# Performance work log

Measured on AMD Instinct MI355X. Metric: run time of the kernel, lower is better.

The kernel has to match this reference:

```python
import jax, jax.numpy as jnp
import numpy as np

def mexican_hat(z):
    z2 = z * z
    return (1.0 - z2) * jnp.exp(-0.5 * z2)

def setup_inputs() -> dict:
    key = jax.random.key(0)
    k1, k2 = jax.random.split(key)
    B, N, D = 8192, 512, 64
    x = jax.random.normal(k1, (B, D), dtype=jnp.float32)
    centers = jax.random.normal(k2, (N, D), dtype=jnp.float32)
    scales = jnp.ones((N, D), dtype=jnp.float32)
    return {"x": x, "centers": centers, "scales": scales}

def reference(x, centers, scales):
    # x: (B, D); centers/scales: (N, D)
    z = (x[:, None, :] - centers[None, :, :]) / scales[None, :, :]  # (B, N, D)
    psi = mexican_hat(z)
    h = jnp.prod(psi, axis=2)  # (B, N)
    return h
```

## Files before the change

kernel.cpp:

```cpp
#include <hip/hip_runtime.h>
#include <hip/hip_bf16.h>


#define DD 64
#define BSTRIP 8

typedef float v2f __attribute__((ext_vector_type(2)));

__global__ __launch_bounds__(256)
void prep(const float* __restrict__ c, const float* __restrict__ s,
          float4* __restrict__ pp, int N) {
    int i = blockIdx.x * 256 + threadIdx.x;
    if (i < (DD / 2) * N) {
        int dp = i / N, n = i - dp * N;
        float r0 = 1.0f / s[n * DD + 2 * dp];
        float r1 = 1.0f / s[n * DD + 2 * dp + 1];
        pp[i] = make_float4(c[n * DD + 2 * dp] * r0,
                            c[n * DD + 2 * dp + 1] * r1, r0, r1);
    }
}

__global__ __launch_bounds__(256, 4)
void wavelet_kernel(const float* __restrict__ x,
                    const float4* __restrict__ pp,
                    float* __restrict__ out, int B, int N) {
    int t = threadIdx.x;
    int lane = t & 63;
    int wv = __builtin_amdgcn_readfirstlane(t >> 6);
    int n = blockIdx.y * 64 + lane;
    int b0 = (blockIdx.x * 4 + wv) * BSTRIP;

    const float4* pcol = pp + n;

    float acc[BSTRIP];
#pragma unroll
    for (int bi = 0; bi < BSTRIP; ++bi) acc[bi] = 1.0f;

#pragma unroll
    for (int h = 0; h < 4; ++h) {
        v2f cp[8], rs[8];
#pragma unroll
        for (int i = 0; i < 8; ++i) {
            float4 q = pcol[(size_t)(h * 8 + i) * N];
            cp[i] = (v2f){q.x, q.y};
            rs[i] = (v2f){q.z, q.w};
        }

#pragma unroll
        for (int bi = 0; bi < BSTRIP; ++bi) {
            const float4* xq =
                (const float4*)(x + (size_t)(b0 + bi) * DD + h * 16);
            float4 X0 = xq[0];
            float4 X1 = xq[1];
            float4 X2 = xq[2];
            float4 X3 = xq[3];
            float xs[16] = {X0.x, X0.y, X0.z, X0.w,
                            X1.x, X1.y, X1.z, X1.w,
                            X2.x, X2.y, X2.z, X2.w,
                            X3.x, X3.y, X3.z, X3.w};
            v2f p  = {1.0f, 1.0f};
            v2f s2 = {0.0f, 0.0f};
#pragma unroll
            for (int k = 0; k < 8; ++k) {
                v2f xv = {xs[2 * k], xs[2 * k + 1]};
                v2f z = __builtin_elementwise_fma(xv, rs[k], -cp[k]);
                v2f w = z * z;
                p = __builtin_elementwise_fma(-w, p, p);
                s2 += w;
            }
            acc[bi] *= (p.x * p.y) *
                       __builtin_exp2f(-0.72134752f * (s2.x + s2.y));
        }
    }

#pragma unroll
    for (int bi = 0; bi < BSTRIP; ++bi)
        out[(size_t)(b0 + bi) * N + n] = acc[bi];
}

extern "C" void kernel_launch(void* const* d_in, const int* in_sizes, int n_in,
                              void* d_out, int out_size, void* d_ws, size_t ws_size,
                              hipStream_t stream) {
    const float* x = (const float*)d_in[0];
    const float* c = (const float*)d_in[1];
    const float* s = (const float*)d_in[2];
    float* out = (float*)d_out;

    int B = in_sizes[0] / DD;
    int N = in_sizes[1] / DD;

    float4* pp = (float4*)d_ws;

    int total = (DD / 2) * N;
    prep<<<(total + 255) / 256, 256, 0, stream>>>(c, s, pp, N);

    dim3 grid(B / (4 * BSTRIP), N / 64);
    wavelet_kernel<<<grid, 256, 0, stream>>>(x, pp, out, B, N);
}
```

Measured before the change: 85.11 us.

## Stage center/scale params through double-buffered LDS via global_load_lds

Each block now loads the precomputed center/scale pairs through a double-buffered shared-memory stage, filled with global_load_lds, and shares them across its four waves. Previously each wave loaded all 32 float4s per lane straight from global memory. The dimension loop is split into eight chunks of eight dims, each prefetching the next chunk. This removes duplicate global loads and register pressure but adds a __syncthreads per chunk and issues exp2 twice as often (once per 8 dims instead of 16).

Result: slower. 185.4 us (+117.9%).

```diff
diff --git a/kernel.cpp b/kernel.cpp
--- a/kernel.cpp
+++ b/kernel.cpp
@@ -24,50 +24,63 @@
 void wavelet_kernel(const float* __restrict__ x,
                     const float4* __restrict__ pp,
                     float* __restrict__ out, int B, int N) {
+    __shared__ float4 ppt[2][4][64];
+
     int t = threadIdx.x;
     int lane = t & 63;
     int wv = __builtin_amdgcn_readfirstlane(t >> 6);
-    int n = blockIdx.y * 64 + lane;
+    int n0 = blockIdx.y * 64;
+    int n = n0 + lane;
     int b0 = (blockIdx.x * 4 + wv) * BSTRIP;
 
-    const float4* pcol = pp + n;
+#define STAGE(hb, buf)                                                        \
+    {                                                                         \
+        const float4* g = pp + (size_t)((hb) * 4 + wv) * N + n0 + lane;       \
+        __builtin_amdgcn_global_load_lds(                                     \
+            (const __attribute__((address_space(1))) void*)g,                 \
+            (__attribute__((address_space(3))) void*)&ppt[buf][wv][0],        \
+            16, 0, 0);                                                        \
+    }
+
+    STAGE(0, 0);
 
     float acc[BSTRIP];
 #pragma unroll
     for (int bi = 0; bi < BSTRIP; ++bi) acc[bi] = 1.0f;
 
+#define PAIR(PR, XA, XB)                                                      \
+    {                                                                         \
+        v2f xv = {XA, XB};                                                    \
+        v2f cp = {PR.x, PR.y};                                                \
+        v2f rv = {PR.z, PR.w};                                                \
+        v2f z = __builtin_elementwise_fma(xv, rv, -cp);                       \
+        v2f w = z * z;                                                        \
+        p = __builtin_elementwise_fma(-w, p, p);                              \
+        s2 += w;                                                              \
+    }
+
 #pragma unroll
-    for (int h = 0; h < 4; ++h) {
-        v2f cp[8], rs[8];
-#pragma unroll
-        for (int i = 0; i < 8; ++i) {
-            float4 q = pcol[(size_t)(h * 8 + i) * N];
-            cp[i] = (v2f){q.x, q.y};
-            rs[i] = (v2f){q.z, q.w};
-        }
+    for (int hb = 0; hb < 8; ++hb) {
+        __syncthreads();
+        if (hb < 7) STAGE(hb + 1, (hb + 1) & 1);
+
+        float4 pr0 = ppt[hb & 1][0][lane];
+        float4 pr1 = ppt[hb & 1][1][lane];
+        float4 pr2 = ppt[hb & 1][2][lane];
+        float4 pr3 = ppt[hb & 1][3][lane];
 
 #pragma unroll
         for (int bi = 0; bi < BSTRIP; ++bi) {
             const float4* xq =
-                (const float4*)(x + (size_t)(b0 + bi) * DD + h * 16);
+                (const float4*)(x + (size_t)(b0 + bi) * DD + hb * 8);
             float4 X0 = xq[0];
             float4 X1 = xq[1];
-            float4 X2 = xq[2];
-            float4 X3 = xq[3];
-            float xs[16] = {X0.x, X0.y, X0.z, X0.w,
-                            X1.x, X1.y, X1.z, X1.w,
-                            X2.x, X2.y, X2.z, X2.w,
-                            X3.x, X3.y, X3.z, X3.w};
             v2f p  = {1.0f, 1.0f};
             v2f s2 = {0.0f, 0.0f};
-#pragma unroll
-            for (int k = 0; k < 8; ++k) {
-                v2f xv = {xs[2 * k], xs[2 * k + 1]};
-                v2f z = __builtin_elementwise_fma(xv, rs[k], -cp[k]);
-                v2f w = z * z;
-                p = __builtin_elementwise_fma(-w, p, p);
-                s2 += w;
-            }
+            PAIR(pr0, X0.x, X0.y)
+            PAIR(pr1, X0.z, X0.w)
+            PAIR(pr2, X1.x, X1.y)
+            PAIR(pr3, X1.z, X1.w)
             acc[bi] *= (p.x * p.y) *
                        __builtin_exp2f(-0.72134752f * (s2.x + s2.y));
         }
@@ -76,6 +89,8 @@
 #pragma unroll
     for (int bi = 0; bi < BSTRIP; ++bi)
         out[(size_t)(b0 + bi) * N + n] = acc[bi];
+#undef PAIR
+#undef STAGE
 }
 
 extern "C" void kernel_launch(void* const* d_in, const int* in_sizes, int n_in,
```
